# Performance work log

Measured on AMD Instinct MI355X. Metric: run time of the kernel, lower is better.

The kernel has to match this reference:

```python
import jax, jax.numpy as jnp
import numpy as np

NL = 4      # num_hidden_layers
NH = 12     # self-attn heads
CH = 4      # cross-attn heads (hardcoded in module)
S = 4       # speakers per dialog
EPS = 1e-5

def layernorm(x, g, b):
    m = x.mean(-1, keepdims=True)
    v = jnp.mean((x - m) ** 2, axis=-1, keepdims=True)
    return (x - m) * jax.lax.rsqrt(v + EPS) * g + b

def self_mha(x, in_w, in_b, out_w, out_b):
    # x: [B,T,L,H] self-attention over L (the per-turn token axis)
    B, T, L, H = x.shape
    dh = H // NH
    qkv = x @ in_w + in_b                       # [B,T,L,3H]
    q, k, v = jnp.split(qkv, 3, axis=-1)
    q = q.reshape(B, T, L, NH, dh); k = k.reshape(B, T, L, NH, dh); v = v.reshape(B, T, L, NH, dh)
    s = jnp.einsum('btqhd,btkhd->bthqk', q, k) / np.sqrt(dh).astype(x.dtype)
    a = jax.nn.softmax(s, axis=-1)
    o = jnp.einsum('bthqk,btkhd->btqhd', a, v).reshape(B, T, L, H)
    return o @ out_w + out_b

def forward(input_ids, attention_mask, speaker_ids, tok_emb, pos_emb, turn_emb,
            mha_in_w, mha_in_b, mha_out_w, mha_out_b,
            ffn_w1, ffn_b1, ffn_w2, ffn_b2,
            ln1_g, ln1_b, ln2_g, ln2_b,
            gate_w, gate_b, sn_g, sn_b,
            ca_in_w, ca_in_b, ca_out_w, ca_out_b):
    B, T, L = input_ids.shape
    H = tok_emb.shape[1]
    X = tok_emb[input_ids] + pos_emb[jnp.arange(L)][None, None] + turn_emb[jnp.arange(T)][None, :, None]
    mask = attention_mask[..., None].astype(X.dtype)            # [B,T,L,1]
    onehot = (speaker_ids[..., None] == jnp.arange(S)).astype(X.dtype)  # [B,T,S]
    counts = onehot.sum(1)                                      # [B,S]
    M = jnp.zeros((B, S, H), X.dtype)                           # speaker memory
    for l in range(NL):
        m_t = jnp.einsum('bts,bsh->bth', onehot, M)             # gather memory per turn
        h = (X + m_t[:, :, None, :]) * mask                     # mask applied by zeroing inputs (as in source)
        h = self_mha(h, mha_in_w[l], mha_in_b[l], mha_out_w[l], mha_out_b[l])
        h = layernorm(h + X, ln1_g[l], ln1_b[l])
        ffn = jax.nn.gelu(h @ ffn_w1[l] + ffn_b1[l], approximate=False) @ ffn_w2[l] + ffn_b2[l]
        h = layernorm(h + ffn, ln2_g[l], ln2_b[l])
        X = h
        tc = h.mean(2)                                          # token_context [B,T,H]
        # cross-attention: each turn's context queries its dialog's speaker memory
        wq, wk, wv = jnp.split(ca_in_w[l], 3, axis=-1)
        bq, bk, bv = jnp.split(ca_in_b[l], 3)
        dh = H // CH
        q = (tc @ wq + bq).reshape(B, T, CH, dh)
        k = (M @ wk + bk).reshape(B, S, CH, dh)
        v = (M @ wv + bv).reshape(B, S, CH, dh)
        s = jnp.einsum('bthd,bshd->bhts', q, k) / np.sqrt(dh).astype(X.dtype)
        a = jax.nn.softmax(s, axis=-1)
        cc = jnp.einsum('bhts,bshd->bthd', a, v).reshape(B, T, H) @ ca_out_w[l] + ca_out_b[l]
        fused = jnp.concatenate([tc, m_t, cc], axis=-1)         # [B,T,3H]
        upd = layernorm(fused @ gate_w[l] + gate_b[l] + m_t, sn_g[l], sn_b[l])
        # scatter: per-speaker mean over that speaker's turns; untouched speakers keep old memory
        sums = jnp.einsum('bts,bth->bsh', onehot, upd)
        mean = sums / jnp.maximum(counts, 1.0)[..., None]
        M = jnp.where((counts > 0)[..., None], mean, M)
    return X, M

def setup_inputs() -> dict:
    key = jax.random.key(0)
    ks = iter(jax.random.split(key, 32))
    B, T, L, H, F, V, P = 8, 64, 64, 768, 3072, 30522, 512
    n = lambda shape: jax.random.normal(next(ks), shape, jnp.float32) * 0.02
    return {
        'input_ids': jax.random.randint(next(ks), (B, T, L), 0, V, jnp.int32),
        'attention_mask': jax.random.randint(next(ks), (B, T, L), 0, 2, jnp.int32),
        'speaker_ids': jax.random.randint(next(ks), (B, T), 0, S, jnp.int32),
        'tok_emb': n((V, H)), 'pos_emb': n((P, H)), 'turn_emb': n((P, H)),
        'mha_in_w': n((NL, H, 3 * H)), 'mha_in_b': jnp.zeros((NL, 3 * H)),
        'mha_out_w': n((NL, H, H)), 'mha_out_b': jnp.zeros((NL, H)),
        'ffn_w1': n((NL, H, F)), 'ffn_b1': jnp.zeros((NL, F)),
        'ffn_w2': n((NL, F, H)), 'ffn_b2': jnp.zeros((NL, H)),
        'ln1_g': jnp.ones((NL, H)), 'ln1_b': jnp.zeros((NL, H)),
        'ln2_g': jnp.ones((NL, H)), 'ln2_b': jnp.zeros((NL, H)),
        'gate_w': n((NL, 3 * H, H)), 'gate_b': jnp.zeros((NL, H)),
        'sn_g': jnp.ones((NL, H)), 'sn_b': jnp.zeros((NL, H)),
        'ca_in_w': n((NL, H, 3 * H)), 'ca_in_b': jnp.zeros((NL, 3 * H)),
        'ca_out_w': n((NL, H, H)), 'ca_out_b': jnp.zeros((NL, H)),
    }

def reference(input_ids, attention_mask, speaker_ids, tok_emb, pos_emb, turn_emb,
              mha_in_w, mha_in_b, mha_out_w, mha_out_b,
              ffn_w1, ffn_b1, ffn_w2, ffn_b2,
              ln1_g, ln1_b, ln2_g, ln2_b,
              gate_w, gate_b, sn_g, sn_b,
              ca_in_w, ca_in_b, ca_out_w, ca_out_b):
    return forward(input_ids, attention_mask, speaker_ids, tok_emb, pos_emb, turn_emb,
                   mha_in_w, mha_in_b, mha_out_w, mha_out_b,
                   ffn_w1, ffn_b1, ffn_w2, ffn_b2,
                   ln1_g, ln1_b, ln2_g, ln2_b,
                   gate_w, gate_b, sn_g, sn_b,
                   ca_in_w, ca_in_b, ca_out_w, ca_out_b)
```

## Files before the change

### kernel.cpp

```cpp
#include <hip/hip_runtime.h>

using u16 = unsigned short;
using u32 = unsigned int;

#define DI __device__ __forceinline__

typedef __bf16 bf16x8 __attribute__((ext_vector_type(8)));
typedef float  f32x4  __attribute__((ext_vector_type(4)));

DI float b2f(u16 u){ u32 x = ((u32)u) << 16; float f; __builtin_memcpy(&f, &x, 4); return f; }
DI u16 f2b(float f){ __bf16 h = (__bf16)f; u16 r; __builtin_memcpy(&r, &h, 2); return r; }
DI float gelu_fast(float v){
    float u = v * (0.7978845608f + 0.0356774081f * v * v);
    float e = __expf(2.0f * u);
    float t = 1.0f - 2.0f / (e + 1.0f);
    return 0.5f * v * (1.0f + t);
}

#define GLOAD16(g, l) __builtin_amdgcn_global_load_lds( \
    (const __attribute__((address_space(1))) void*)(g), \
    (__attribute__((address_space(3))) void*)(l), 16, 0, 0)

DI bf16x8 ldsr128(const u16* p) {
    bf16x8 r;
    asm volatile("ds_read_b128 %0, %1"
                 : "=v"(r)
                 : "v"((const __attribute__((address_space(3))) u16*)p));
    return r;
}

template<int EPI>
__global__ __launch_bounds__(256)
void gemm_bt(const u16* __restrict__ A, const u16* __restrict__ Bt,
             const float* __restrict__ bias, void* __restrict__ Cout,
             int M, int N, int K)
{
    __shared__ u16 lA[3][128 * 32];
    __shared__ u16 lB[3][128 * 32];
    const int tid  = threadIdx.x;
    const int lane = tid & 63;
    const int w    = tid >> 6;
    const int wm   = w >> 1, wn = w & 1;

    const int nx = gridDim.x;
    const int nb = nx * gridDim.y;
    int bid = blockIdx.y * nx + blockIdx.x;
    if ((nb & 7) == 0) bid = ((bid & 7) * (nb >> 3)) + (bid >> 3);
    const int m0 = (bid / nx) * 128;
    const int n0 = (bid % nx) * 128;

    f32x4 acc[4][4] = {};

    const int srow = tid >> 2;
    const int scol = (((tid & 3) ^ ((tid >> 3) & 3)) * 8);
    int ar0 = m0 + srow;      if (ar0 > M - 1) ar0 = M - 1;
    int ar1 = m0 + 64 + srow; if (ar1 > M - 1) ar1 = M - 1;
    const u16* gA0 = A  + (size_t)ar0 * K + scol;
    const u16* gA1 = A  + (size_t)ar1 * K + scol;
    const u16* gB0 = Bt + (size_t)(n0 + srow) * K + scol;
    const u16* gB1 = Bt + (size_t)(n0 + 64 + srow) * K + scol;

    const int la = lane & 15, lg = lane >> 4;
    const int cp = (lg ^ ((la >> 1) & 3)) * 8;

    const int nt = K >> 5;

    GLOAD16(gA0,      &lA[0][tid * 8]);
    GLOAD16(gA1,      &lA[0][tid * 8 + 2048]);
    GLOAD16(gB0,      &lB[0][tid * 8]);
    GLOAD16(gB1,      &lB[0][tid * 8 + 2048]);
    GLOAD16(gA0 + 32, &lA[1][tid * 8]);
    GLOAD16(gA1 + 32, &lA[1][tid * 8 + 2048]);
    GLOAD16(gB0 + 32, &lB[1][tid * 8]);
    GLOAD16(gB1 + 32, &lB[1][tid * 8 + 2048]);

    int cur = 0, pre = 2;
    for (int t = 0; t < nt; ++t) {
        if (t + 1 < nt) asm volatile("s_waitcnt vmcnt(4)" ::: "memory");
        else            asm volatile("s_waitcnt vmcnt(0)" ::: "memory");
        __builtin_amdgcn_s_barrier();
        asm volatile("" ::: "memory");

        if (t + 2 < nt) {
            const int k0 = (t + 2) << 5;
            GLOAD16(gA0 + k0, &lA[pre][tid * 8]);
            GLOAD16(gA1 + k0, &lA[pre][tid * 8 + 2048]);
            GLOAD16(gB0 + k0, &lB[pre][tid * 8]);
            GLOAD16(gB1 + k0, &lB[pre][tid * 8 + 2048]);
        }

        bf16x8 af[4], bfr[4];
        #pragma unroll
        for (int i = 0; i < 4; i++)
            af[i] = ldsr128(&lA[cur][(wm * 64 + i * 16 + la) * 32 + cp]);
        #pragma unroll
        for (int j = 0; j < 4; j++)
            bfr[j] = ldsr128(&lB[cur][(wn * 64 + j * 16 + la) * 32 + cp]);
        asm volatile("s_waitcnt lgkmcnt(0)" ::: "memory");
        __builtin_amdgcn_sched_barrier(0);

        #pragma unroll
        for (int i = 0; i < 4; i++)
            #pragma unroll
            for (int j = 0; j < 4; j++)
                acc[i][j] = __builtin_amdgcn_mfma_f32_16x16x32_bf16(af[i], bfr[j], acc[i][j], 0, 0, 0);

        cur = (cur == 2) ? 0 : cur + 1;
        pre = (pre == 2) ? 0 : pre + 1;
    }

    #pragma unroll
    for (int i = 0; i < 4; i++) {
        const int rowb = m0 + wm * 64 + i * 16 + lg * 4;
        #pragma unroll
        for (int j = 0; j < 4; j++) {
            const int col = n0 + wn * 64 + j * 16 + la;
            const float bv = bias[col];
            #pragma unroll
            for (int r = 0; r < 4; r++) {
                const int rr = rowb + r;
                if (rr < M) {
                    float v = acc[i][j][r] + bv;
                    if constexpr (EPI == 1) v = gelu_fast(v);
                    if constexpr (EPI == 2) ((float*)Cout)[(size_t)rr * N + col] = v;
                    else                    ((u16*)Cout)[(size_t)rr * N + col] = f2b(v);
                }
            }
        }
    }
}

__global__ __launch_bounds__(256)
void transp_conv(const float* __restrict__ in, u16* __restrict__ out, int K, int N)
{
    __shared__ float tile[32][33];
    const int l = blockIdx.z;
    const float* inp = in + (size_t)l * K * N;
    u16* op = out + (size_t)l * K * N;
    const int kb = blockIdx.y * 32, nb = blockIdx.x * 32;
    const int tx = threadIdx.x, ty = threadIdx.y;
    #pragma unroll
    for (int i = 0; i < 32; i += 8)
        tile[ty + i][tx] = inp[(size_t)(kb + ty + i) * N + nb + tx];
    __syncthreads();
    #pragma unroll
    for (int i = 0; i < 32; i += 8)
        op[(size_t)(nb + ty + i) * K + kb + tx] = f2b(tile[tx][ty + i]);
}

__global__ __launch_bounds__(192)
void embed_k(const int* __restrict__ ids, const float* __restrict__ te,
             const float* __restrict__ pe, const float* __restrict__ ue,
             u16* __restrict__ X)
{
    const int tok = blockIdx.x;
    const int l = tok & 63;
    const int t = (tok >> 6) & 63;
    const int id = ids[tok];
    const int c = threadIdx.x * 4;
    float4 a = *(const float4*)&te[(size_t)id * 768 + c];
    float4 p = *(const float4*)&pe[(size_t)l * 768 + c];
    float4 u = *(const float4*)&ue[(size_t)t * 768 + c];
    ushort4 o;
    o.x = f2b(a.x + p.x + u.x); o.y = f2b(a.y + p.y + u.y);
    o.z = f2b(a.z + p.z + u.z); o.w = f2b(a.w + p.w + u.w);
    *(ushort4*)&X[(size_t)tok * 768 + c] = o;
}

__global__ __launch_bounds__(256)
void gather_mt(const float* __restrict__ M, const int* __restrict__ sid,
               float* __restrict__ mt)
{
    const int bt = blockIdx.x, b = bt >> 6, tid = threadIdx.x;
    const float* src = M + ((size_t)b * 4 + sid[bt]) * 768;
    float* dst = mt + (size_t)bt * 768;
    dst[tid] = src[tid]; dst[tid + 256] = src[tid + 256]; dst[tid + 512] = src[tid + 512];
}

__global__ __launch_bounds__(192)
void prep_ain(const u16* __restrict__ X, const float* __restrict__ mt,
              const int* __restrict__ mask, u16* __restrict__ Ain)
{
    const int tok = blockIdx.x, bt = tok >> 6;
    const float mk = (float)mask[tok];
    const int c = threadIdx.x * 4;
    ushort4 xv = *(const ushort4*)&X[(size_t)tok * 768 + c];
    float4 mv = *(const float4*)&mt[(size_t)bt * 768 + c];
    ushort4 o;
    o.x = f2b((b2f(xv.x) + mv.x) * mk); o.y = f2b((b2f(xv.y) + mv.y) * mk);
    o.z = f2b((b2f(xv.z) + mv.z) * mk); o.w = f2b((b2f(xv.w) + mv.w) * mk);
    *(ushort4*)&Ain[(size_t)tok * 768 + c] = o;
}

DI int swz(int row, int col) { return row * 64 + (((col >> 3) ^ (row & 7)) << 3) + (col & 7); }

__global__ __launch_bounds__(256)
void attn_self(const u16* __restrict__ QKV, u16* __restrict__ O)
{
    __shared__ u16 lQ[64 * 64], lK[64 * 64], lVt[64 * 64], lP[64 * 64];
    __shared__ float lS[64 * 68];
    const int bt = blockIdx.x / 12, h = blockIdx.x % 12;
    const int tid = threadIdx.x, lane = tid & 63, w = tid >> 6;
    const size_t base = (size_t)bt * 64 * 2304;

    #pragma unroll
    for (int it = 0; it < 2; ++it) {
        const int slot = it * 256 + tid;
        const int l = slot >> 3, dc = (slot & 7) * 8;
        const u16* qp = QKV + base + (size_t)l * 2304 + h * 64 + dc;
        *(uint4*)&lQ[swz(l, dc)] = *(const uint4*)qp;
        *(uint4*)&lK[swz(l, dc)] = *(const uint4*)(qp + 768);
        uint4 vv = *(const uint4*)(qp + 1536);
        u16 tmp[8]; *(uint4*)tmp = vv;
        #pragma unroll
        for (int j = 0; j < 8; j++) lVt[swz(dc + j, l)] = tmp[j];
    }
    __syncthreads();

    const int la = lane & 15, lg = lane >> 4;
    {
        f32x4 sa[4] = {};
        #pragma unroll
        for (int kh = 0; kh < 64; kh += 32) {
            bf16x8 aq = *(const bf16x8*)&lQ[swz(w * 16 + la, kh + lg * 8)];
            #pragma unroll
            for (int fn = 0; fn < 4; ++fn) {
                bf16x8 bk = *(const bf16x8*)&lK[swz(fn * 16 + la, kh + lg * 8)];
                sa[fn] = __builtin_amdgcn_mfma_f32_16x16x32_bf16(aq, bk, sa[fn], 0, 0, 0);
            }
        }
        #pragma unroll
        for (int fn = 0; fn < 4; ++fn)
            #pragma unroll
            for (int r = 0; r < 4; ++r)
                lS[(w * 16 + lg * 4 + r) * 68 + fn * 16 + la] = sa[fn][r] * 0.125f;
    }
    __syncthreads();

    {
        const int row = tid >> 2, q4 = tid & 3;
        float e[16]; float mx = -1e30f;
        #pragma unroll
        for (int j = 0; j < 16; j++) { e[j] = lS[row * 68 + q4 * 16 + j]; mx = fmaxf(mx, e[j]); }
        mx = fmaxf(mx, __shfl_xor(mx, 1)); mx = fmaxf(mx, __shfl_xor(mx, 2));
        float sm = 0.f;
        #pragma unroll
        for (int j = 0; j < 16; j++) { e[j] = __expf(e[j] - mx); sm += e[j]; }
        sm += __shfl_xor(sm, 1); sm += __shfl_xor(sm, 2);
        const float inv = 1.0f / sm;
        #pragma unroll
        for (int j = 0; j < 16; j++) lP[swz(row, q4 * 16 + j)] = f2b(e[j] * inv);
    }
    __syncthreads();

    {
        f32x4 oa[4] = {};
        #pragma unroll
        for (int kh = 0; kh < 64; kh += 32) {
            bf16x8 ap = *(const bf16x8*)&lP[swz(w * 16 + la, kh + lg * 8)];
            #pragma unroll
            for (int fn = 0; fn < 4; ++fn) {
                bf16x8 bv = *(const bf16x8*)&lVt[swz(fn * 16 + la, kh + lg * 8)];
                oa[fn] = __builtin_amdgcn_mfma_f32_16x16x32_bf16(ap, bv, oa[fn], 0, 0, 0);
            }
        }
        const size_t ob = (size_t)bt * 64 * 768 + h * 64;
        #pragma unroll
        for (int fn = 0; fn < 4; ++fn)
            #pragma unroll
            for (int r = 0; r < 4; ++r)
                O[ob + (size_t)(w * 16 + lg * 4 + r) * 768 + fn * 16 + la] = f2b(oa[fn][r]);
    }
}

DI float wave_red(float v) {
    #pragma unroll
    for (int o = 32; o > 0; o >>= 1) v += __shfl_xor(v, o);
    return v;
}

__global__ __launch_bounds__(256)
void ln_res(const u16* __restrict__ a, const u16* __restrict__ b,
            const float* __restrict__ g, const float* __restrict__ be,
            u16* __restrict__ out)
{
    __shared__ float red[8];
    const int tid = threadIdx.x;
    const size_t off = (size_t)blockIdx.x * 768;
    float x0 = b2f(a[off + tid])       + b2f(b[off + tid]);
    float x1 = b2f(a[off + tid + 256]) + b2f(b[off + tid + 256]);
    float x2 = b2f(a[off + tid + 512]) + b2f(b[off + tid + 512]);
    float s = wave_red(x0 + x1 + x2);
    float ss = wave_red(x0 * x0 + x1 * x1 + x2 * x2);
    if ((tid & 63) == 0) { red[tid >> 6] = s; red[4 + (tid >> 6)] = ss; }
    __syncthreads();
    s = red[0] + red[1] + red[2] + red[3];
    ss = red[4] + red[5] + red[6] + red[7];
    const float mean = s * (1.f / 768.f);
    const float var = fmaxf(ss * (1.f / 768.f) - mean * mean, 0.f);
    const float inv = rsqrtf(var + 1e-5f);
    out[off + tid]       = f2b((x0 - mean) * inv * g[tid]       + be[tid]);
    out[off + tid + 256] = f2b((x1 - mean) * inv * g[tid + 256] + be[tid + 256]);
    out[off + tid + 512] = f2b((x2 - mean) * inv * g[tid + 512] + be[tid + 512]);
}

__global__ __launch_bounds__(256)
void ln_upd(const float* __restrict__ a, const float* __restrict__ b,
            const float* __restrict__ g, const float* __restrict__ be,
            float* __restrict__ out)
{
    __shared__ float red[8];
    const int tid = threadIdx.x;
    const size_t off = (size_t)blockIdx.x * 768;
    float x0 = a[off + tid]       + b[off + tid];
    float x1 = a[off + tid + 256] + b[off + tid + 256];
    float x2 = a[off + tid + 512] + b[off + tid + 512];
    float s = wave_red(x0 + x1 + x2);
    float ss = wave_red(x0 * x0 + x1 * x1 + x2 * x2);
    if ((tid & 63) == 0) { red[tid >> 6] = s; red[4 + (tid >> 6)] = ss; }
    __syncthreads();
    s = red[0] + red[1] + red[2] + red[3];
    ss = red[4] + red[5] + red[6] + red[7];
    const float mean = s * (1.f / 768.f);
    const float var = fmaxf(ss * (1.f / 768.f) - mean * mean, 0.f);
    const float inv = rsqrtf(var + 1e-5f);
    out[off + tid]       = (x0 - mean) * inv * g[tid]       + be[tid];
    out[off + tid + 256] = (x1 - mean) * inv * g[tid + 256] + be[tid + 256];
    out[off + tid + 512] = (x2 - mean) * inv * g[tid + 512] + be[tid + 512];
}

__global__ __launch_bounds__(256)
void tc_mean(const u16* __restrict__ X, u16* __restrict__ tcb)
{
    const int bt = blockIdx.x, tid = threadIdx.x;
    float s0 = 0, s1 = 0, s2 = 0;
    for (int l = 0; l < 64; ++l) {
        const u16* r = X + ((size_t)bt * 64 + l) * 768;
        s0 += b2f(r[tid]); s1 += b2f(r[tid + 256]); s2 += b2f(r[tid + 512]);
    }
    tcb[(size_t)bt * 768 + tid]       = f2b(s0 * (1.f / 64.f));
    tcb[(size_t)bt * 768 + tid + 256] = f2b(s1 * (1.f / 64.f));
    tcb[(size_t)bt * 768 + tid + 512] = f2b(s2 * (1.f / 64.f));
}

__global__ __launch_bounds__(256)
void conv_bf16(const float* __restrict__ in, u16* __restrict__ out, int n)
{
    const int i = blockIdx.x * 256 + threadIdx.x;
    if (i < n) out[i] = f2b(in[i]);
}

__global__ __launch_bounds__(256)
void zero_f32(float* __restrict__ buf, int n)
{
    const int i = blockIdx.x * 256 + threadIdx.x;
    if (i < n) buf[i] = 0.f;
}

__global__ __launch_bounds__(256)
void cross_attn(const u16* __restrict__ qc, const u16* __restrict__ kvc,
                u16* __restrict__ cca)
{
    __shared__ float q[768], kk[4][768], vv[4][768], sraw[16], aw[16];
    const int bt = blockIdx.x, b = bt >> 6, tid = threadIdx.x;
    #pragma unroll
    for (int i = 0; i < 3; i++) q[tid + i * 256] = b2f(qc[(size_t)bt * 768 + tid + i * 256]);
    #pragma unroll
    for (int i = 0; i < 12; i++) {
        const int idx = i * 256 + tid;
        const int s = idx / 768, d = idx % 768;
        kk[s][d] = b2f(kvc[(size_t)(b * 4 + s) * 1536 + d]);
        vv[s][d] = b2f(kvc[(size_t)(b * 4 + s) * 1536 + 768 + d]);
    }
    __syncthreads();
    if (tid < 16) {
        const int hh = tid >> 2, s = tid & 3;
        float acc = 0.f;
        for (int d = 0; d < 192; ++d) acc += q[hh * 192 + d] * kk[s][hh * 192 + d];
        sraw[tid] = acc * 0.07216878364870323f;
    }
    __syncthreads();
    if (tid < 4) {
        float m = -1e30f;
        for (int s = 0; s < 4; s++) m = fmaxf(m, sraw[tid * 4 + s]);
        float ee[4], sm = 0.f;
        for (int s = 0; s < 4; s++) { ee[s] = __expf(sraw[tid * 4 + s] - m); sm += ee[s]; }
        for (int s = 0; s < 4; s++) aw[tid * 4 + s] = ee[s] / sm;
    }
    __syncthreads();
    #pragma unroll
    for (int i = 0; i < 3; i++) {
        const int j = tid + i * 256;
        const int hh = j / 192;
        float v = aw[hh * 4 + 0] * vv[0][j] + aw[hh * 4 + 1] * vv[1][j]
                + aw[hh * 4 + 2] * vv[2][j] + aw[hh * 4 + 3] * vv[3][j];
        cca[(size_t)bt * 768 + j] = f2b(v);
    }
}

__global__ __launch_bounds__(256)
void concat_fused(const u16* __restrict__ tcb, const float* __restrict__ mt,
                  const u16* __restrict__ ccp, u16* __restrict__ Fu)
{
    const int bt = blockIdx.x, tid = threadIdx.x;
    u16* o = Fu + (size_t)bt * 2304;
    #pragma unroll
    for (int i = 0; i < 3; i++) {
        const int j = tid + i * 256;
        o[j]        = tcb[(size_t)bt * 768 + j];
        o[768 + j]  = f2b(mt[(size_t)bt * 768 + j]);
        o[1536 + j] = ccp[(size_t)bt * 768 + j];
    }
}

__global__ __launch_bounds__(256)
void scatter_mem(const float* __restrict__ upd, const int* __restrict__ sid,
                 const float* __restrict__ counts, float* __restrict__ M)
{
    const int bs = blockIdx.x, b = bs >> 2, s = bs & 3, tid = threadIdx.x;
    const float c = counts[bs];
    #pragma unroll
    for (int i = 0; i < 3; i++) {
        const int j = tid + i * 256;
        float acc = 0.f;
        for (int t = 0; t < 64; ++t)
            if (sid[b * 64 + t] == s) acc += upd[((size_t)b * 64 + t) * 768 + j];
        if (c > 0.f) M[(size_t)bs * 768 + j] = acc / fmaxf(c, 1.f);
    }
}

__global__ void calc_counts(const int* __restrict__ sid, float* __restrict__ counts)
{
    const int tid = threadIdx.x;
    if (tid < 32) {
        const int b = tid >> 2, s = tid & 3;
        float c = 0.f;
        for (int t = 0; t < 64; ++t) c += (sid[b * 64 + t] == s) ? 1.f : 0.f;
        counts[tid] = c;
    }
}

__global__ __launch_bounds__(256)
void final_out(const u16* __restrict__ Xb, const float* __restrict__ M,
               float* __restrict__ out)
{
    const size_t i = (size_t)blockIdx.x * 256 + threadIdx.x;
    const size_t NX = 25165824ull;
    if (i < NX) out[i] = b2f(Xb[i]);
    else if (i < NX + 24576ull) out[i] = M[i - NX];
}

extern "C" void kernel_launch(void* const* d_in, const int* in_sizes, int n_in,
                              void* d_out, int out_size, void* d_ws, size_t ws_size,
                              hipStream_t stream)
{
    const int*   input_ids = (const int*)d_in[0];
    const int*   attn_mask = (const int*)d_in[1];
    const int*   sid       = (const int*)d_in[2];
    const float* tok_emb   = (const float*)d_in[3];
    const float* pos_emb   = (const float*)d_in[4];
    const float* turn_emb  = (const float*)d_in[5];
    const float* mha_in_w  = (const float*)d_in[6];
    const float* mha_in_b  = (const float*)d_in[7];
    const float* mha_out_w = (const float*)d_in[8];
    const float* mha_out_b = (const float*)d_in[9];
    const float* ffn_w1    = (const float*)d_in[10];
    const float* ffn_b1    = (const float*)d_in[11];
    const float* ffn_w2    = (const float*)d_in[12];
    const float* ffn_b2    = (const float*)d_in[13];
    const float* ln1_g     = (const float*)d_in[14];
    const float* ln1_b     = (const float*)d_in[15];
    const float* ln2_g     = (const float*)d_in[16];
    const float* ln2_b     = (const float*)d_in[17];
    const float* gate_w    = (const float*)d_in[18];
    const float* gate_b    = (const float*)d_in[19];
    const float* sn_g      = (const float*)d_in[20];
    const float* sn_b      = (const float*)d_in[21];
    const float* ca_in_w   = (const float*)d_in[22];
    const float* ca_in_b   = (const float*)d_in[23];
    const float* ca_out_w  = (const float*)d_in[24];
    const float* ca_out_b  = (const float*)d_in[25];
    (void)in_sizes; (void)n_in; (void)out_size;

    const size_t MB = 1ull << 20;
    int NCA, NCF; bool allW;
    if      (ws_size >= 460 * MB) { NCA = 2; NCF = 1; allW = true;  }
    else if (ws_size >= 255 * MB) { NCA = 2; NCF = 2; allW = false; }
    else                          { NCA = 4; NCF = 4; allW = false; }
    const int MRA = 32768 / NCA;
    const int MRF = 32768 / NCF;
    const size_t wl = allW ? 4 : 1;

    char* p = (char*)d_ws;
    auto alloc = [&](size_t n) { void* r = p; p += (n + 255) & ~(size_t)255; return r; };
    u16*   Xb    = (u16*)alloc(50331648);
    u16*   Hb    = (u16*)alloc(50331648);
    u16*   WqkvT = (u16*)alloc(wl * 3538944);
    u16*   WoT   = (u16*)alloc(wl * 1179648);
    u16*   W1T   = (u16*)alloc(wl * 4718592);
    u16*   W2T   = (u16*)alloc(wl * 4718592);
    u16*   WgT   = (u16*)alloc(wl * 3538944);
    u16*   WcaT  = (u16*)alloc(wl * 3538944);
    u16*   WcoT  = (u16*)alloc(wl * 1179648);
    float* mt    = (float*)alloc(1572864);
    u16*   tcb   = (u16*)alloc(786432);
    u16*   Mb    = (u16*)alloc(49152);
    u16*   qc    = (u16*)alloc(786432);
    u16*   kvc   = (u16*)alloc(98304);
    u16*   cca   = (u16*)alloc(786432);
    u16*   ccp   = (u16*)alloc(786432);
    u16*   Fu    = (u16*)alloc(2359296);
    float* gout  = (float*)alloc(1572864);
    float* upd   = (float*)alloc(1572864);
    float* cnts  = (float*)alloc(256);
    float* M     = (float*)alloc(98304);

    u16 *A, *QKVb, *Gb;
    if (NCF == 1) {
        A    = (u16*)alloc(50331648);
        Gb   = (u16*)alloc(201326592);
        QKVb = (u16*)d_out;
    } else if (NCF == 2) {
        A    = (u16*)alloc(50331648);
        QKVb = (u16*)alloc((size_t)MRA * 2304 * 2);
        Gb   = (u16*)d_out;
    } else {
        Gb   = (u16*)alloc((size_t)MRF * 3072 * 2);
        A    = (u16*)d_out;
        QKVb = (u16*)d_out + 25165824;
    }
    u16* Obuf = Gb;

    zero_f32<<<96, 256, 0, stream>>>(M, 24576);
    calc_counts<<<1, 64, 0, stream>>>(sid, cnts);
    embed_k<<<32768, 192, 0, stream>>>(input_ids, tok_emb, pos_emb, turn_emb, Xb);

    if (allW) {
        transp_conv<<<dim3(72, 24, 4), dim3(32, 8), 0, stream>>>(mha_in_w,  WqkvT, 768, 2304);
        transp_conv<<<dim3(24, 24, 4), dim3(32, 8), 0, stream>>>(mha_out_w, WoT,   768, 768);
        transp_conv<<<dim3(96, 24, 4), dim3(32, 8), 0, stream>>>(ffn_w1,    W1T,   768, 3072);
        transp_conv<<<dim3(24, 96, 4), dim3(32, 8), 0, stream>>>(ffn_w2,    W2T,  3072, 768);
        transp_conv<<<dim3(24, 72, 4), dim3(32, 8), 0, stream>>>(gate_w,    WgT,  2304, 768);
        transp_conv<<<dim3(72, 24, 4), dim3(32, 8), 0, stream>>>(ca_in_w,   WcaT,  768, 2304);
        transp_conv<<<dim3(24, 24, 4), dim3(32, 8), 0, stream>>>(ca_out_w,  WcoT,  768, 768);
    }

    for (int l = 0; l < 4; ++l) {
        if (!allW) {
            transp_conv<<<dim3(72, 24), dim3(32, 8), 0, stream>>>(mha_in_w  + (size_t)l * 768 * 2304, WqkvT, 768, 2304);
            transp_conv<<<dim3(24, 24), dim3(32, 8), 0, stream>>>(mha_out_w + (size_t)l * 768 * 768,  WoT,   768, 768);
            transp_conv<<<dim3(96, 24), dim3(32, 8), 0, stream>>>(ffn_w1    + (size_t)l * 768 * 3072, W1T,   768, 3072);
            transp_conv<<<dim3(24, 96), dim3(32, 8), 0, stream>>>(ffn_w2    + (size_t)l * 3072 * 768, W2T,  3072, 768);
            transp_conv<<<dim3(24, 72), dim3(32, 8), 0, stream>>>(gate_w    + (size_t)l * 2304 * 768, WgT,  2304, 768);
            transp_conv<<<dim3(72, 24), dim3(32, 8), 0, stream>>>(ca_in_w   + (size_t)l * 768 * 2304, WcaT,  768, 2304);
            transp_conv<<<dim3(24, 24), dim3(32, 8), 0, stream>>>(ca_out_w  + (size_t)l * 768 * 768,  WcoT,  768, 768);
        }
        const u16* Wqkv_l = WqkvT + (size_t)(allW ? l : 0) * 2304 * 768;
        const u16* Wo_l   = WoT   + (size_t)(allW ? l : 0) * 768 * 768;
        const u16* W1_l   = W1T   + (size_t)(allW ? l : 0) * 768 * 3072;
        const u16* W2_l   = W2T   + (size_t)(allW ? l : 0) * 3072 * 768;
        const u16* Wg_l   = WgT   + (size_t)(allW ? l : 0) * 2304 * 768;
        const u16* Wca_l  = WcaT  + (size_t)(allW ? l : 0) * 768 * 2304;
        const u16* Wco_l  = WcoT  + (size_t)(allW ? l : 0) * 768 * 768;

        gather_mt<<<512, 256, 0, stream>>>(M, sid, mt);
        prep_ain<<<32768, 192, 0, stream>>>(Xb, mt, attn_mask, A);

        for (int c = 0; c < NCA; ++c) {
            u16* Ac = A + (size_t)c * MRA * 768;
            gemm_bt<0><<<dim3(18, MRA / 128), 256, 0, stream>>>(Ac, Wqkv_l, mha_in_b + l * 2304, QKVb, MRA, 2304, 768);
            attn_self<<<(MRA / 64) * 12, 256, 0, stream>>>(QKVb, Obuf);
            gemm_bt<0><<<dim3(6, MRA / 128), 256, 0, stream>>>(Obuf, Wo_l, mha_out_b + l * 768, Ac, MRA, 768, 768);
        }
        ln_res<<<32768, 256, 0, stream>>>(A, Xb, ln1_g + l * 768, ln1_b + l * 768, Hb);

        for (int c = 0; c < NCF; ++c) {
            u16* Hc = Hb + (size_t)c * MRF * 768;
            u16* Ac = A  + (size_t)c * MRF * 768;
            gemm_bt<1><<<dim3(24, MRF / 128), 256, 0, stream>>>(Hc, W1_l, ffn_b1 + l * 3072, Gb, MRF, 3072, 768);
            gemm_bt<0><<<dim3(6, MRF / 128), 256, 0, stream>>>(Gb, W2_l, ffn_b2 + l * 768, Ac, MRF, 768, 3072);
        }
        ln_res<<<32768, 256, 0, stream>>>(A, Hb, ln2_g + l * 768, ln2_b + l * 768, Xb);

        tc_mean<<<512, 256, 0, stream>>>(Xb, tcb);
        conv_bf16<<<96, 256, 0, stream>>>(M, Mb, 24576);
        gemm_bt<0><<<dim3(6, 4), 256, 0, stream>>>(tcb, Wca_l, ca_in_b + l * 2304, qc, 512, 768, 768);
        gemm_bt<0><<<dim3(12, 1), 256, 0, stream>>>(Mb, Wca_l + 768 * 768, ca_in_b + l * 2304 + 768, kvc, 32, 1536, 768);
        cross_attn<<<512, 256, 0, stream>>>(qc, kvc, cca);
        gemm_bt<0><<<dim3(6, 4), 256, 0, stream>>>(cca, Wco_l, ca_out_b + l * 768, ccp, 512, 768, 768);
        concat_fused<<<512, 256, 0, stream>>>(tcb, mt, ccp, Fu);
        gemm_bt<2><<<dim3(6, 4), 256, 0, stream>>>(Fu, Wg_l, gate_b + l * 768, gout, 512, 768, 2304);
        ln_upd<<<512, 256, 0, stream>>>(gout, mt, sn_g + l * 768, sn_b + l * 768, upd);
        scatter_mem<<<32, 256, 0, stream>>>(upd, sid, cnts, M);
    }

    final_out<<<98400, 256, 0, stream>>>(Xb, M, (float*)d_out);
}
```

Before: 4.067 ms.

## Add 256x256-tile GEMM kernel for the large self-attention and FFN projections

```diff
diff --git a/kernel.cpp b/kernel.cpp
--- a/kernel.cpp
+++ b/kernel.cpp
@@ -27,6 +27,105 @@
                  : "=v"(r)
                  : "v"((const __attribute__((address_space(3))) u16*)p));
     return r;
+}
+
+template<int EPI>
+__global__ __launch_bounds__(512, 2)
+void gemm256(const u16* __restrict__ A, const u16* __restrict__ Bt,
+             const float* __restrict__ bias, void* __restrict__ Cout,
+             int M, int N, int K)
+{
+    __shared__ u16 lA[3][256 * 32];
+    __shared__ u16 lB[3][256 * 32];
+    const int tid  = threadIdx.x;
+    const int lane = tid & 63;
+    const int w    = tid >> 6;
+    const int wm   = w >> 2, wn = w & 3;
+
+    const int nx = gridDim.x;
+    const int nb = nx * gridDim.y;
+    int bid = blockIdx.y * nx + blockIdx.x;
+    if ((nb & 7) == 0) bid = ((bid & 7) * (nb >> 3)) + (bid >> 3);
+    const int m0 = (bid / nx) * 256;
+    const int n0 = (bid % nx) * 256;
+
+    f32x4 acc[8][4] = {};
+
+    const int srow = tid >> 2;
+    const int scol = (((tid & 3) ^ ((tid >> 3) & 3)) * 8);
+    int ar0 = m0 + srow;       if (ar0 > M - 1) ar0 = M - 1;
+    int ar1 = m0 + 128 + srow; if (ar1 > M - 1) ar1 = M - 1;
+    const u16* gA0 = A  + (size_t)ar0 * K + scol;
+    const u16* gA1 = A  + (size_t)ar1 * K + scol;
+    const u16* gB0 = Bt + (size_t)(n0 + srow) * K + scol;
+    const u16* gB1 = Bt + (size_t)(n0 + 128 + srow) * K + scol;
+
+    const int la = lane & 15, lg = lane >> 4;
+    const int cp = (lg ^ ((la >> 1) & 3)) * 8;
+
+    const int nt = K >> 5;
+
+    #define STAGE256(buf, koff) do { \
+        GLOAD16(gA0 + (koff), &lA[buf][tid * 8]); \
+        GLOAD16(gA1 + (koff), &lA[buf][4096 + tid * 8]); \
+        GLOAD16(gB0 + (koff), &lB[buf][tid * 8]); \
+        GLOAD16(gB1 + (koff), &lB[buf][4096 + tid * 8]); \
+    } while (0)
+
+    STAGE256(0, 0);
+    STAGE256(1, 32);
+
+    int cur = 0, pre = 2;
+    for (int t = 0; t < nt; ++t) {
+        if (t + 1 < nt) asm volatile("s_waitcnt vmcnt(4)" ::: "memory");
+        else            asm volatile("s_waitcnt vmcnt(0)" ::: "memory");
+        __builtin_amdgcn_s_barrier();
+        asm volatile("" ::: "memory");
+
+        if (t + 2 < nt) STAGE256(pre, (t + 2) << 5);
+
+        bf16x8 af[8], bfr[4];
+        #pragma unroll
+        for (int i = 0; i < 8; i++)
+            af[i] = ldsr128(&lA[cur][(wm * 128 + i * 16 + la) * 32 + cp]);
+        #pragma unroll
+        for (int j = 0; j < 4; j++)
+            bfr[j] = ldsr128(&lB[cur][(wn * 64 + j * 16 + la) * 32 + cp]);
+        asm volatile("s_waitcnt lgkmcnt(0)" ::: "memory");
+        __builtin_amdgcn_sched_barrier(0);
+
+        __builtin_amdgcn_s_setprio(1);
+        #pragma unroll
+        for (int i = 0; i < 8; i++)
+            #pragma unroll
+            for (int j = 0; j < 4; j++)
+                acc[i][j] = __builtin_amdgcn_mfma_f32_16x16x32_bf16(af[i], bfr[j], acc[i][j], 0, 0, 0);
+        __builtin_amdgcn_s_setprio(0);
+
+        cur = (cur == 2) ? 0 : cur + 1;
+        pre = (pre == 2) ? 0 : pre + 1;
+    }
+    #undef STAGE256
+
+    #pragma unroll
+    for (int i = 0; i < 8; i++) {
+        const int rowb = m0 + wm * 128 + i * 16 + lg * 4;
+        #pragma unroll
+        for (int j = 0; j < 4; j++) {
+            const int col = n0 + wn * 64 + j * 16 + la;
+            const float bv = bias[col];
+            #pragma unroll
+            for (int r = 0; r < 4; r++) {
+                const int rr = rowb + r;
+                if (rr < M) {
+                    float v = acc[i][j][r] + bv;
+                    if constexpr (EPI == 1) v = gelu_fast(v);
+                    if constexpr (EPI == 2) ((float*)Cout)[(size_t)rr * N + col] = v;
+                    else                    ((u16*)Cout)[(size_t)rr * N + col] = f2b(v);
+                }
+            }
+        }
+    }
 }
 
 template<int EPI>
@@ -568,17 +667,17 @@
 
         for (int c = 0; c < NCA; ++c) {
             u16* Ac = A + (size_t)c * MRA * 768;
-            gemm_bt<0><<<dim3(18, MRA / 128), 256, 0, stream>>>(Ac, Wqkv_l, mha_in_b + l * 2304, QKVb, MRA, 2304, 768);
+            gemm256<0><<<dim3(9, MRA / 256), 512, 0, stream>>>(Ac, Wqkv_l, mha_in_b + l * 2304, QKVb, MRA, 2304, 768);
             attn_self<<<(MRA / 64) * 12, 256, 0, stream>>>(QKVb, Obuf);
-            gemm_bt<0><<<dim3(6, MRA / 128), 256, 0, stream>>>(Obuf, Wo_l, mha_out_b + l * 768, Ac, MRA, 768, 768);
+            gemm256<0><<<dim3(3, MRA / 256), 512, 0, stream>>>(Obuf, Wo_l, mha_out_b + l * 768, Ac, MRA, 768, 768);
         }
         ln_res<<<32768, 256, 0, stream>>>(A, Xb, ln1_g + l * 768, ln1_b + l * 768, Hb);
 
         for (int c = 0; c < NCF; ++c) {
             u16* Hc = Hb + (size_t)c * MRF * 768;
             u16* Ac = A  + (size_t)c * MRF * 768;
-            gemm_bt<1><<<dim3(24, MRF / 128), 256, 0, stream>>>(Hc, W1_l, ffn_b1 + l * 3072, Gb, MRF, 3072, 768);
-            gemm_bt<0><<<dim3(6, MRF / 128), 256, 0, stream>>>(Gb, W2_l, ffn_b2 + l * 768, Ac, MRF, 768, 3072);
+            gemm256<1><<<dim3(12, MRF / 256), 512, 0, stream>>>(Hc, W1_l, ffn_b1 + l * 3072, Gb, MRF, 3072, 768);
+            gemm256<0><<<dim3(3, MRF / 256), 512, 0, stream>>>(Gb, W2_l, ffn_b2 + l * 768, Ac, MRF, 768, 3072);
         }
         ln_res<<<32768, 256, 0, stream>>>(A, Hb, ln2_g + l * 768, ln2_b + l * 768, Xb);
 
```

Result: slower. 4.256 ms (+4.6%).
